# Kernel optimization log

Measured on AMD Instinct MI355X. Metric: run time of the kernel, lower is better.

The kernel has to match this reference:

```python
import jax, jax.numpy as jnp
import numpy as np

FM = 128       # feature_maps
QM = 128       # query_maps
ROUNDS = 4     # test_rounds (training=False)
N_VARS = 24576
N_CLAUSES = 98304
N_EDGES = 3 * N_CLAUSES
EPS = 1e-6


def _dense(k, fan_in, fan_out):
    return jax.random.normal(k, (fan_in, fan_out), jnp.float32) * (1.0 / np.sqrt(fan_in))


def setup_inputs() -> dict:
    key = jax.random.key(0)
    ks = jax.random.split(key, 20)
    return {
        "edge_lit": jax.random.randint(ks[0], (N_EDGES,), 0, 2 * N_VARS, dtype=jnp.int32),
        "edge_clause": jnp.sort(jax.random.randint(ks[1], (N_EDGES,), 0, N_CLAUSES, dtype=jnp.int32)),
        "noise_v": jax.random.normal(ks[2], (ROUNDS, N_VARS, 4), jnp.float32),
        "noise_c": jax.random.normal(ks[3], (ROUNDS, N_CLAUSES, 4), jnp.float32),
        # variables_query: MLP(2, QM, QM), input FM+4
        "vq_w0": _dense(ks[4], FM + 4, QM), "vq_b0": jnp.zeros((QM,), jnp.float32),
        "vq_w1": _dense(ks[5], QM, QM),     "vq_b1": jnp.zeros((QM,), jnp.float32),
        # clauses_query: MLP(2, QM, QM), input FM+4
        "cq_w0": _dense(ks[6], FM + 4, QM), "cq_b0": jnp.zeros((QM,), jnp.float32),
        "cq_w1": _dense(ks[7], QM, QM),     "cq_b1": jnp.zeros((QM,), jnp.float32),
        # clause_update: MLP(2, 2*FM, FM+QM), input FM+2*QM=384
        "cm_w0": _dense(ks[8], FM + 2 * QM, 2 * FM), "cm_b0": jnp.zeros((2 * FM,), jnp.float32),
        "cm_w1": _dense(ks[9], 2 * FM, FM + QM),     "cm_b1": jnp.zeros((FM + QM,), jnp.float32),
        # update_gate: MLP(3, 2*FM, FM), input QM+FM+2*QM=512
        "ug_w0": _dense(ks[10], QM + FM + 2 * QM, 2 * FM), "ug_b0": jnp.zeros((2 * FM,), jnp.float32),
        "ug_w1": _dense(ks[11], 2 * FM, 2 * FM),           "ug_b1": jnp.zeros((2 * FM,), jnp.float32),
        "ug_w2": _dense(ks[12], 2 * FM, FM),               "ug_b2": jnp.zeros((FM,), jnp.float32),
        # clauses_mask_output: MLP(2, FM, 1)
        "co_w0": _dense(ks[13], FM, FM), "co_b0": jnp.zeros((FM,), jnp.float32),
        "co_w1": _dense(ks[14], FM, 1),  "co_b1": jnp.zeros((1,), jnp.float32),
        "n_vars": N_VARS,
        "n_clauses": N_CLAUSES,
    }


def _forward(edge_lit, edge_clause, n_vars, n_clauses, floats):
    (noise_v, noise_c,
     vq_w0, vq_b0, vq_w1, vq_b1,
     cq_w0, cq_b0, cq_w1, cq_b1,
     cm_w0, cm_b0, cm_w1, cm_b1,
     ug_w0, ug_b0, ug_w1, ug_b1, ug_w2, ug_b2,
     co_w0, co_b0, co_w1, co_b1) = floats

    n_edges = edge_lit.shape[0]
    # lit_degree = row sums of sparse adjacency (all nonzeros are 1.0)
    lit_degree = jax.ops.segment_sum(jnp.ones((n_edges,), jnp.float32), edge_lit,
                                     num_segments=2 * n_vars)[:, None]          # [2V,1]
    degree_weight = jax.lax.rsqrt(jnp.maximum(lit_degree, 1.0))
    var_degree_weight = 4.0 * jax.lax.rsqrt(
        jnp.maximum(lit_degree[:n_vars] + lit_degree[n_vars:], 1.0))            # [V,1]

    def mlp2(x, w0, b0, w1, b1):
        return jax.nn.relu(x @ w0 + b0) @ w1 + b1

    def mlp3(x, w0, b0, w1, b1, w2, b2):
        h = jax.nn.relu(x @ w0 + b0)
        h = jax.nn.relu(h @ w1 + b1)
        return h @ w2 + b2

    def pair_norm(x):
        # PairNorm(subtract_mean=True), single graph -> global mean over nodes
        x = x - jnp.mean(x, axis=0, keepdims=True)
        return x * jax.lax.rsqrt(jnp.mean(jnp.square(x)) + EPS)

    def clauses_loss_fn(vq, cq):
        # unsat_cnf_clauses_loss: softplus literal values aggregated per clause,
        # clause satisfiability exp(-sum), gated by clause query mask.
        lits = jax.nn.softplus(jnp.concatenate([vq, -vq], axis=0))              # [2V,Q]
        csum = jax.ops.segment_sum(lits[edge_lit], edge_clause,
                                   num_segments=n_clauses)                      # [C,Q]
        loss = jnp.exp(-csum) * jax.nn.sigmoid(cq)
        return jnp.mean(loss), loss

    grad_fn = jax.grad(clauses_loss_fn, argnums=(0, 1), has_aux=True)

    def step(carry, xs):
        variables, clauses = carry
        nv, nc = xs
        vq = mlp2(jnp.concatenate([variables, nv], -1), vq_w0, vq_b0, vq_w1, vq_b1)
        cq = mlp2(jnp.concatenate([clauses, nc], -1), cq_w0, cq_b0, cq_w1, cq_b1)
        (vgrad, cgrad), clauses_loss = grad_fn(vq, cq)
        vgrad = vgrad * var_degree_weight
        clauses_loss = clauses_loss * 4.0
        clause_data = mlp2(jnp.concatenate([clauses, clauses_loss, cgrad], -1),
                           cm_w0, cm_b0, cm_w1, cm_b1)                          # [C,FM+QM]
        variables_loss_all = clause_data[:, :QM]
        clauses = pair_norm(clause_data[:, QM:]) * 0.25 + 0.1 * clauses
        # adj_matrix @ variables_loss_all (literal-side aggregation)
        variables_loss = jax.ops.segment_sum(variables_loss_all[edge_clause], edge_lit,
                                             num_segments=2 * n_vars) * degree_weight
        unit = jnp.concatenate([vgrad, variables,
                                variables_loss[:n_vars], variables_loss[n_vars:]], -1)
        variables = pair_norm(mlp3(unit, ug_w0, ug_b0, ug_w1, ug_b1, ug_w2, ug_b2)) * 0.25 \
                    + 0.1 * variables
        logits = mlp2(clauses, co_w0, co_b0, co_w1, co_b1)[:, 0]                # [C]
        return (variables, clauses), logits

    init = (jnp.ones((n_vars, FM), jnp.float32), jnp.ones((n_clauses, FM), jnp.float32))
    _, logits = jax.lax.scan(step, init, (noise_v, noise_c))                    # [R,C]
    return jax.nn.sigmoid(logits), jax.nn.softplus(logits)


def reference(edge_lit, edge_clause, noise_v, noise_c,
              vq_w0, vq_b0, vq_w1, vq_b1,
              cq_w0, cq_b0, cq_w1, cq_b1,
              cm_w0, cm_b0, cm_w1, cm_b1,
              ug_w0, ug_b0, ug_w1, ug_b1, ug_w2, ug_b2,
              co_w0, co_b0, co_w1, co_b1,
              n_vars, n_clauses):
    floats = (noise_v, noise_c,
              vq_w0, vq_b0, vq_w1, vq_b1,
              cq_w0, cq_b0, cq_w1, cq_b1,
              cm_w0, cm_b0, cm_w1, cm_b1,
              ug_w0, ug_b0, ug_w1, ug_b1, ug_w2, ug_b2,
              co_w0, co_b0, co_w1, co_b1)
    return _forward(edge_lit, edge_clause, int(n_vars), int(n_clauses), floats)
```

## Files before the change

### kernel.cpp

```cpp
#include <hip/hip_runtime.h>
#include <math.h>

#define NV 24576
#define NC 98304
#define NE 294912
#define CMCHUNK 24576

typedef unsigned short bf16;
typedef _Float16 f16;
using bf8 = __attribute__((ext_vector_type(8))) short;
using f4  = __attribute__((ext_vector_type(4))) float;

static constexpr float INV_CQM = 1.0f / 12582912.0f;
static constexpr float LOG2E = 1.44269504f;
static constexpr float LN2 = 0.69314718f;

__device__ __forceinline__ float b2f(bf16 h) { return __uint_as_float(((unsigned)h) << 16); }
__device__ __forceinline__ bf16 f2b(float f) {
  unsigned u = __float_as_uint(f);
  u += 0x7fff + ((u >> 16) & 1);
  return (bf16)(u >> 16);
}
__device__ __forceinline__ float fexp2(float x) { float r; asm("v_exp_f32 %0, %1" : "=v"(r) : "v"(x)); return r; }
__device__ __forceinline__ float flog2(float x) { float r; asm("v_log_f32 %0, %1" : "=v"(r) : "v"(x)); return r; }
__device__ __forceinline__ float frcpf(float x) { float r; asm("v_rcp_f32 %0, %1" : "=v"(r) : "v"(x)); return r; }
__device__ __forceinline__ float fsigm(float x) { return frcpf(1.0f + fexp2(-x * LOG2E)); }
__device__ __forceinline__ float fsoftplus(float x) {
  return fmaxf(x, 0.0f) + LN2 * flog2(1.0f + fexp2(-fabsf(x) * LOG2E));
}
__device__ __forceinline__ float cvt_ld(float x) { return x; }
__device__ __forceinline__ float cvt_ld(bf16 x) { return b2f(x); }

__device__ __forceinline__ void gload16(const void* g, void* l) {
  __builtin_amdgcn_global_load_lds((const __attribute__((address_space(1))) unsigned int*)g,
                                   (__attribute__((address_space(3))) unsigned int*)l, 16, 0, 0);
}


__global__ __launch_bounds__(256) void k_cptr(const int* __restrict__ ec, int* __restrict__ ptr) {
  int c = blockIdx.x * 256 + threadIdx.x;
  if (c > NC) return;
  int lo = 0, hi = NE;
  while (lo < hi) { int mid = (lo + hi) >> 1; if (ec[mid] < c) lo = mid + 1; else hi = mid; }
  ptr[c] = lo;
}

__global__ __launch_bounds__(256) void k_litcnt(const int* __restrict__ el, int* __restrict__ cnt) {
  int e = blockIdx.x * 256 + threadIdx.x;
  atomicAdd(&cnt[el[e]], 1);
}

__global__ __launch_bounds__(1024) void k_scan(int* __restrict__ cnt, int* __restrict__ ptr) {
  __shared__ int wsum[16];
  __shared__ int carry_s;
  int tid = threadIdx.x, lane = tid & 63, w = tid >> 6;
  if (tid == 0) carry_s = 0;
  __syncthreads();
  for (int base = 0; base < 2 * NV; base += 1024) {
    int x = cnt[base + tid];
    int v = x;
#pragma unroll
    for (int off = 1; off < 64; off <<= 1) {
      int y = __shfl_up(v, off, 64);
      if (lane >= off) v += y;
    }
    if (lane == 63) wsum[w] = v;
    __syncthreads();
    int carry = carry_s;
    int wpre = 0;
    for (int i = 0; i < w; ++i) wpre += wsum[i];
    int excl = carry + wpre + (v - x);
    ptr[base + tid] = excl;
    cnt[base + tid] = excl;
    __syncthreads();
    if (tid == 1023) carry_s = carry + wpre + v;
  }
  __syncthreads();
  if (tid == 0) ptr[2 * NV] = carry_s;
}

__global__ __launch_bounds__(256) void k_fillsort(const int* __restrict__ el, const int* __restrict__ ec,
                                                  int* __restrict__ cur, int* __restrict__ lclause) {
  int e = blockIdx.x * 256 + threadIdx.x;
  int pos = atomicAdd(&cur[el[e]], 1);
  lclause[pos] = ec[e];
}

__global__ __launch_bounds__(256) void k_degree(const int* __restrict__ lptr, float* __restrict__ dw,
                                                float* __restrict__ vdw) {
  int l = blockIdx.x * 256 + threadIdx.x;
  if (l < 2 * NV) dw[l] = rsqrtf(fmaxf((float)(lptr[l + 1] - lptr[l]), 1.0f));
  if (l < NV) {
    int d = (lptr[l + 1] - lptr[l]) + (lptr[l + NV + 1] - lptr[l + NV]);
    vdw[l] = 4.0f * rsqrtf(fmaxf((float)d, 1.0f));
  }
}

__global__ __launch_bounds__(256) void k_init_v(float* __restrict__ variables, bf16* __restrict__ ugA) {
  int i = blockIdx.x * 256 + threadIdx.x;
  variables[i] = 1.0f;
  ugA[(size_t)(i >> 7) * 512 + 128 + (i & 127)] = 0x3F80;
}
__global__ __launch_bounds__(256) void k_init_c(bf16* __restrict__ cmA) {
  int i = blockIdx.x * 256 + threadIdx.x;
  cmA[(size_t)(i >> 7) * 256 + (i & 127)] = 0x3F80;
}

__global__ __launch_bounds__(256) void k_wt(const float* __restrict__ w, bf16* __restrict__ wt,
                                            int K, int N, int Kpad) {
  int idx = blockIdx.x * 256 + threadIdx.x;
  int n = idx / Kpad, k = idx % Kpad;
  if (n >= N) return;
  wt[idx] = (k < K) ? f2b(w[(size_t)k * N + n]) : (bf16)0;
}


struct GP {
  const bf16* A0; const bf16* A1; int lda;
  const float* noise; const bf16* WT; const float* Bv;
  void* o0; void* o1; int ldOut;
};

enum { AL_STD = 0, AL_NOISE = 1, AL_CM = 2 };

template <int KDIM, int AL, bool RELU, int OUT>
__device__ __forceinline__ void gemm_body(const GP g, int bx, char* smem) {
  constexpr int NT = KDIM / 64;
  const int tid = threadIdx.x;
  const int m0 = bx * 128;
  const int n0 = blockIdx.y * 128;
  const int lane = tid & 63;
  const int w = tid >> 6;
  const int wr = w >> 1, wc = w & 1;
  const int rl = (tid >> 3) & 7;
  const int cc = tid & 7;
  const int swzoff = (cc * 16) ^ (rl << 4);

  auto stage = [&](int t, int buf) {
    char* As = smem + buf * 32768;
    char* Bs = As + 16384;
    const int k0 = t * 64;
    if (AL == AL_NOISE && t == 2) {
      const int srow = tid >> 3, schunk = tid & 7;
#pragma unroll
      for (int it = 0; it < 4; ++it) {
        int row = srow + it * 32;
        alignas(16) bf16 tmp[8];
#pragma unroll
        for (int e = 0; e < 8; ++e) {
          int kk = schunk * 8 + e;
          tmp[e] = (kk < 4) ? f2b(g.noise[(size_t)(m0 + row) * 4 + kk]) : (bf16)0;
        }
        *reinterpret_cast<uint4*>(&As[row * 128 + ((schunk * 16) ^ ((row & 7) << 4))]) =
            *reinterpret_cast<uint4*>(tmp);
        int row0 = it * 32 + w * 8;
        gload16((const char*)(g.WT + (size_t)(n0 + row0 + rl) * KDIM + k0) + swzoff, Bs + row0 * 128);
      }
    } else {
      const bf16* Ap = g.A0;
      int co_ = k0;
      if (AL == AL_CM) {
        if (t >= 2 && t < 4) Ap = g.A1;
        if (t >= 2) co_ = k0 - 128;
      }
#pragma unroll
      for (int it = 0; it < 4; ++it) {
        int row0 = it * 32 + w * 8;
        int row = row0 + rl;
        gload16((const char*)(Ap + (size_t)(m0 + row) * g.lda + co_) + swzoff, As + row0 * 128);
        gload16((const char*)(g.WT + (size_t)(n0 + row) * KDIM + k0) + swzoff, Bs + row0 * 128);
      }
    }
  };

  f4 acc[4][4] = {};
  stage(0, 0);
#pragma unroll
  for (int t = 0; t < NT; ++t) {
    const int buf = t & 1;
    __builtin_amdgcn_sched_barrier(0);
    if (t + 1 < NT) {
      stage(t + 1, buf ^ 1);
      if (AL == AL_NOISE && t + 1 == 2) {
        asm volatile("s_waitcnt vmcnt(4) lgkmcnt(0)" ::: "memory");
      } else {
        asm volatile("s_waitcnt vmcnt(8) lgkmcnt(0)" ::: "memory");
      }
    } else {
      asm volatile("s_waitcnt vmcnt(0) lgkmcnt(0)" ::: "memory");
    }
    __builtin_amdgcn_s_barrier();
    __builtin_amdgcn_sched_barrier(0);
    const char* As = smem + buf * 32768;
    const char* Bs = As + 16384;
#pragma unroll
    for (int kk = 0; kk < 2; ++kk) {
      bf8 a[4], b[4];
#pragma unroll
      for (int i = 0; i < 4; ++i) {
        int r = wr * 64 + i * 16 + (lane & 15);
        int cby = (kk * 64 + ((lane >> 4) * 16)) ^ ((r & 7) << 4);
        a[i] = *reinterpret_cast<const bf8*>(&As[r * 128 + cby]);
        int c = wc * 64 + i * 16 + (lane & 15);
        int cby2 = (kk * 64 + ((lane >> 4) * 16)) ^ ((c & 7) << 4);
        b[i] = *reinterpret_cast<const bf8*>(&Bs[c * 128 + cby2]);
      }
#pragma unroll
      for (int i = 0; i < 4; ++i)
#pragma unroll
        for (int j = 0; j < 4; ++j)
          acc[i][j] = __builtin_amdgcn_mfma_f32_16x16x32_bf16(a[i], b[j], acc[i][j], 0, 0, 0);
    }
    __builtin_amdgcn_sched_barrier(0);
    __builtin_amdgcn_s_barrier();
  }
  const int colloc = wc * 64 + (lane & 15);
  const int rowbase = m0 + wr * 64 + ((lane >> 4) << 2);

  if constexpr (OUT == 4) {
    const float* w1 = (const float*)g.o1;
    float* outp = (float*)g.o0;
    const int t = g.ldOut;
    float part[4][4];
#pragma unroll
    for (int i = 0; i < 4; ++i)
#pragma unroll
      for (int p = 0; p < 4; ++p) part[i][p] = 0.0f;
#pragma unroll
    for (int j = 0; j < 4; ++j) {
      int c = colloc + j * 16;
      float bias = g.Bv[c];
      float w1c = w1[c];
#pragma unroll
      for (int i = 0; i < 4; ++i)
#pragma unroll
        for (int p = 0; p < 4; ++p)
          part[i][p] += fmaxf(acc[i][j][p] + bias, 0.0f) * w1c;
    }
#pragma unroll
    for (int m = 1; m < 16; m <<= 1)
#pragma unroll
      for (int i = 0; i < 4; ++i)
#pragma unroll
        for (int p = 0; p < 4; ++p)
          part[i][p] += __shfl_xor(part[i][p], m, 64);
    float* red = (float*)smem;
    if ((lane & 15) == 0) {
#pragma unroll
      for (int i = 0; i < 4; ++i)
#pragma unroll
        for (int p = 0; p < 4; ++p)
          red[wc * 128 + wr * 64 + i * 16 + ((lane >> 4) << 2) + p] = part[i][p];
    }
    __syncthreads();
    if (tid < 128) {
      float lg = red[tid] + red[128 + tid] + g.noise[0];
      int row = m0 + tid;
      outp[(size_t)t * NC + row] = fsigm(lg);
      outp[(size_t)4 * NC + (size_t)t * NC + row] = fsoftplus(lg);
    }
    return;
  }

#pragma unroll
  for (int j = 0; j < 4; ++j) {
    int c = n0 + colloc + j * 16;
    float bias = g.Bv[c];
#pragma unroll
    for (int i = 0; i < 4; ++i) {
      int rb = rowbase + i * 16;
#pragma unroll
      for (int p = 0; p < 4; ++p) {
        float v = acc[i][j][p] + bias;
        if (RELU) v = fmaxf(v, 0.0f);
        int r = rb + p;
        if constexpr (OUT == 0) {
          ((float*)g.o0)[(size_t)r * g.ldOut + c] = v;
        } else if constexpr (OUT == 1) {
          ((bf16*)g.o0)[(size_t)r * g.ldOut + c] = f2b(v);
        } else if constexpr (OUT == 2) {
          if (c < 128) ((bf16*)g.o0)[(size_t)r * 256 + c] = f2b(v);
          else ((bf16*)g.o1)[(size_t)r * 128 + (c - 128)] = f2b(v);
        } else {
          float tq = LN2 * flog2(1.0f + fexp2(-fabsf(v) * LOG2E));
          ((f16*)g.o0)[(size_t)r * 128 + c] = (f16)(fmaxf(v, 0.0f) + tq);
          ((f16*)g.o1)[(size_t)r * 128 + c] = (f16)(fmaxf(-v, 0.0f) + tq);
        }
      }
    }
  }
}

template <int KDIM, int AL, bool RELU, int OUT>
__global__ __launch_bounds__(256) void mgemm_s(GP g) {
  __shared__ __align__(16) char smem[65536];
  gemm_body<KDIM, AL, RELU, OUT>(g, blockIdx.x, smem);
}

template <int KDIM, int AL, bool RELU, int OUTA, int OUTB>
__global__ __launch_bounds__(256) void mgemm_d(GP ga, GP gb, int nA) {
  __shared__ __align__(16) char smem[65536];
  if ((int)blockIdx.x < nA) gemm_body<KDIM, AL, RELU, OUTA>(ga, blockIdx.x, smem);
  else gemm_body<KDIM, AL, RELU, OUTB>(gb, blockIdx.x - nA, smem);
}


__global__ __launch_bounds__(256) void k_loss(const int* __restrict__ edge_lit, const int* __restrict__ cptr,
                                              const f16* __restrict__ sp, bf16* __restrict__ gbuf,
                                              bf16* __restrict__ cmA) {
  const int g = threadIdx.x >> 7;
  const int q = threadIdx.x & 127;
  const int c0 = blockIdx.x * 16 + g * 8;
#pragma unroll
  for (int ci = 0; ci < 8; ++ci) {
    int c = c0 + ci;
    int e0 = cptr[c], e1 = cptr[c + 1];
    float csum = 0.0f;
    for (int e = e0; e < e1; e += 4) {
#pragma unroll
      for (int k = 0; k < 4; ++k) {
        int ee = e + k;
        bool ok = ee < e1;
        int lit = ok ? edge_lit[ee] : 0;
        float v = ok ? (float)sp[(size_t)lit * 128 + q] : 0.0f;
        csum += v;
      }
    }
    float s = fsigm(b2f(gbuf[(size_t)c * 256 + 128 + q]));
    float L = fexp2(-csum * LOG2E) * s;
    gbuf[(size_t)c * 256 + q] = f2b(4.0f * L);
    cmA[(size_t)c * 256 + 128 + q] = f2b(L * (1.0f - s) * INV_CQM);
  }
}

__global__ __launch_bounds__(256) void k_gatherv(const int* __restrict__ lptr, const int* __restrict__ lclause,
                                                 const bf16* __restrict__ gbuf, const f16* __restrict__ spn,
                                                 const float* __restrict__ dw, const float* __restrict__ vdw,
                                                 bf16* __restrict__ ugA) {
  int v = blockIdx.x;
  int half = threadIdx.x >> 7, q = threadIdx.x & 127;
  int l = v + half * NV;
  int j0 = lptr[l], j1 = lptr[l + 1];
  float sg = 0.0f, sv = 0.0f;
  for (int j = j0; j < j1; j += 4) {
#pragma unroll
    for (int k = 0; k < 4; ++k) {
      int jj = j + k;
      bool ok = jj < j1;
      int c = ok ? lclause[jj] : 0;
      float a = ok ? b2f(gbuf[(size_t)c * 256 + q]) : 0.0f;
      float b = ok ? b2f(gbuf[(size_t)c * 256 + 128 + q]) : 0.0f;
      sg += a;
      sv += b;
    }
  }
  __shared__ float sgl[2][128];
  sgl[half][q] = sg;
  ugA[(size_t)v * 512 + 256 + half * 128 + q] = f2b(sv * dw[l]);
  __syncthreads();
  if (half == 0) {
    float s = fexp2(-LOG2E * (float)spn[(size_t)v * 128 + q]);
    float g = ((1.0f - s) * sgl[1][q] - s * sgl[0][q]) * (INV_CQM * 0.25f) * vdw[v];
    ugA[(size_t)v * 512 + q] = f2b(g);
  }
}

template <typename T>
__global__ __launch_bounds__(256) void k_pn_stats(const T* __restrict__ X, int R, float* __restrict__ stats) {
  int q = threadIdx.x & 127;
  int rg = threadIdx.x >> 7;
  float cs = 0.0f, ss = 0.0f;
  for (int r = blockIdx.x * 2 + rg; r < R; r += gridDim.x * 2) {
    float x = cvt_ld(X[(size_t)r * 128 + q]);
    cs += x;
    ss += x * x;
  }
  __shared__ float scs[256], sss[256];
  scs[threadIdx.x] = cs;
  sss[threadIdx.x] = ss;
  __syncthreads();
  if (threadIdx.x < 128) atomicAdd(&stats[q], scs[q] + scs[128 + q]);
  for (int off = 128; off; off >>= 1) {
    if (threadIdx.x < off) sss[threadIdx.x] += sss[threadIdx.x + off];
    __syncthreads();
  }
  if (threadIdx.x == 0) atomicAdd(&stats[128], sss[0]);
}

__global__ __launch_bounds__(128) void k_pn_final(float* __restrict__ stats, float R) {
  __shared__ float s[128];
  int q = threadIdx.x;
  float m = stats[q] / R;
  s[q] = m * m;
  __syncthreads();
  for (int off = 64; off; off >>= 1) {
    if (q < off) s[q] += s[q + off];
    __syncthreads();
  }
  if (q == 0) {
    float var = (stats[128] - R * s[0]) / (R * 128.0f);
    stats[129] = rsqrtf(fmaxf(var, 0.0f) + 1e-6f) * 0.25f;
  }
  stats[q] = m;
}

__global__ __launch_bounds__(256) void k_pn_apply_c(const bf16* __restrict__ cd1, const float* __restrict__ stats,
                                                    bf16* __restrict__ cmA) {
  int i = blockIdx.x * 256 + threadIdx.x;
  int c = i >> 7, q = i & 127;
  float x = b2f(cd1[i]);
  float old = b2f(cmA[(size_t)c * 256 + q]);
  cmA[(size_t)c * 256 + q] = f2b((x - stats[q]) * stats[129] + 0.1f * old);
}

__global__ __launch_bounds__(256) void k_pn_apply_v(const float* __restrict__ uout, const float* __restrict__ stats,
                                                    float* __restrict__ variables, bf16* __restrict__ ugA) {
  int i = blockIdx.x * 256 + threadIdx.x;
  int v = i >> 7, q = i & 127;
  float nv = (uout[i] - stats[q]) * stats[129] + 0.1f * variables[i];
  variables[i] = nv;
  ugA[(size_t)v * 512 + 128 + q] = f2b(nv);
}


extern "C" void kernel_launch(void* const* d_in, const int* in_sizes, int n_in,
                              void* d_out, int out_size, void* d_ws, size_t ws_size,
                              hipStream_t stream) {
  const int* edge_lit = (const int*)d_in[0];
  const int* edge_clause = (const int*)d_in[1];
  const float* noise_v = (const float*)d_in[2];
  const float* noise_c = (const float*)d_in[3];
  const float* vq_w0 = (const float*)d_in[4];  const float* vq_b0 = (const float*)d_in[5];
  const float* vq_w1 = (const float*)d_in[6];  const float* vq_b1 = (const float*)d_in[7];
  const float* cq_w0 = (const float*)d_in[8];  const float* cq_b0 = (const float*)d_in[9];
  const float* cq_w1 = (const float*)d_in[10]; const float* cq_b1 = (const float*)d_in[11];
  const float* cm_w0 = (const float*)d_in[12]; const float* cm_b0 = (const float*)d_in[13];
  const float* cm_w1 = (const float*)d_in[14]; const float* cm_b1 = (const float*)d_in[15];
  const float* ug_w0 = (const float*)d_in[16]; const float* ug_b0 = (const float*)d_in[17];
  const float* ug_w1 = (const float*)d_in[18]; const float* ug_b1 = (const float*)d_in[19];
  const float* ug_w2 = (const float*)d_in[20]; const float* ug_b2 = (const float*)d_in[21];
  const float* co_w0 = (const float*)d_in[22]; const float* co_b0 = (const float*)d_in[23];
  const float* co_w1 = (const float*)d_in[24]; const float* co_b1 = (const float*)d_in[25];
  float* out = (float*)d_out;

  char* base = (char*)d_ws;
  size_t off = 0;
  auto A = [&](size_t n) -> char* {
    char* p = base + off;
    off = (off + n + 255) & ~(size_t)255;
    return p;
  };
  float* variables = (float*)A((size_t)NV * 128 * 4);
  bf16* cmA        = (bf16*)A((size_t)NC * 256 * 2);
  bf16* gbuf       = (bf16*)A((size_t)NC * 256 * 2);
  bf16* ugA        = (bf16*)A((size_t)NV * 512 * 2);
  char* R_h        = A((size_t)NC * 128 * 2);
  char* R_big      = A((size_t)2 * NV * 128 * 2 + (size_t)NV * 128 * 4);
  bf16* wtb        = (bf16*)A(983424);
  int* cptr = (int*)A((size_t)(NC + 1) * 4);
  int* lptr = (int*)A((size_t)(2 * NV + 1) * 4);
  int* lcur = (int*)A((size_t)2 * NV * 4);
  int* lclause = (int*)A((size_t)NE * 4);
  float* dw  = (float*)A((size_t)2 * NV * 4);
  float* vdw = (float*)A((size_t)NV * 4);
  float* stats = (float*)A(2048);
  if (off > ws_size) {
    hipMemsetAsync(d_out, 0xFF, (size_t)out_size * 4, stream);
    return;
  }

  bf16* hc  = (bf16*)R_h;
  bf16* cd1 = (bf16*)R_h;
  bf16* uh1 = (bf16*)R_h;
  bf16* uh2 = (bf16*)(R_h + (size_t)NV * 256 * 2);
  bf16* hv  = (bf16*)R_big;
  bf16* cmh = (bf16*)R_big;
  f16* spp  = (f16*)(R_big + 12582912);
  f16* spn  = spp + (size_t)NV * 128;
  float* uout = (float*)(R_big + 12582912);

  size_t wo = 0;
  auto WTa = [&](int n, int kp) { bf16* p = wtb + wo; wo += (size_t)n * kp; return p; };
  bf16* wt_vq0 = WTa(128, 192); bf16* wt_vq1 = WTa(128, 128);
  bf16* wt_cq0 = WTa(128, 192); bf16* wt_cq1 = WTa(128, 128);
  bf16* wt_cm0 = WTa(256, 384); bf16* wt_cm1 = WTa(256, 256);
  bf16* wt_ug0 = WTa(256, 512); bf16* wt_ug1 = WTa(256, 256);
  bf16* wt_ug2 = WTa(128, 256); bf16* wt_co0 = WTa(128, 128);

  hipMemsetAsync(lcur, 0, (size_t)2 * NV * 4, stream);
  k_cptr<<<(NC + 256) / 256, 256, 0, stream>>>(edge_clause, cptr);
  k_litcnt<<<NE / 256, 256, 0, stream>>>(edge_lit, lcur);
  k_scan<<<1, 1024, 0, stream>>>(lcur, lptr);
  k_fillsort<<<NE / 256, 256, 0, stream>>>(edge_lit, edge_clause, lcur, lclause);
  k_degree<<<(2 * NV + 255) / 256, 256, 0, stream>>>(lptr, dw, vdw);
  k_init_v<<<NV * 128 / 256, 256, 0, stream>>>(variables, ugA);
  k_init_c<<<NC * 128 / 256, 256, 0, stream>>>(cmA);
  k_wt<<<128 * 192 / 256, 256, 0, stream>>>(vq_w0, wt_vq0, 132, 128, 192);
  k_wt<<<128 * 128 / 256, 256, 0, stream>>>(vq_w1, wt_vq1, 128, 128, 128);
  k_wt<<<128 * 192 / 256, 256, 0, stream>>>(cq_w0, wt_cq0, 132, 128, 192);
  k_wt<<<128 * 128 / 256, 256, 0, stream>>>(cq_w1, wt_cq1, 128, 128, 128);
  k_wt<<<256 * 384 / 256, 256, 0, stream>>>(cm_w0, wt_cm0, 384, 256, 384);
  k_wt<<<256 * 256 / 256, 256, 0, stream>>>(cm_w1, wt_cm1, 256, 256, 256);
  k_wt<<<256 * 512 / 256, 256, 0, stream>>>(ug_w0, wt_ug0, 512, 256, 512);
  k_wt<<<256 * 256 / 256, 256, 0, stream>>>(ug_w1, wt_ug1, 256, 256, 256);
  k_wt<<<128 * 256 / 256, 256, 0, stream>>>(ug_w2, wt_ug2, 256, 128, 256);
  k_wt<<<128 * 128 / 256, 256, 0, stream>>>(co_w0, wt_co0, 128, 128, 128);

  for (int t = 0; t < 4; ++t) {
    const float* nvp = noise_v + (size_t)t * NV * 4;
    const float* ncp = noise_c + (size_t)t * NC * 4;
    {
      GP pa{ugA + 128, nullptr, 512, nvp, wt_vq0, vq_b0, hv, nullptr, 128};
      GP pb{cmA, nullptr, 256, ncp, wt_cq0, cq_b0, hc, nullptr, 128};
      mgemm_d<192, AL_NOISE, true, 1, 1><<<dim3(960, 1), 256, 0, stream>>>(pa, pb, 192);
    }
    {
      GP pa{hv, nullptr, 128, nullptr, wt_vq1, vq_b1, spp, spn, 128};
      GP pb{hc, nullptr, 128, nullptr, wt_cq1, cq_b1, gbuf + 128, nullptr, 256};
      mgemm_d<128, AL_STD, false, 3, 1><<<dim3(960, 1), 256, 0, stream>>>(pa, pb, 192);
    }
    k_loss<<<NC / 16, 256, 0, stream>>>(edge_lit, cptr, spp, gbuf, cmA);
    for (int ch = 0; ch < NC / CMCHUNK; ++ch) {
      size_t ro = (size_t)ch * CMCHUNK;
      GP p0{cmA + ro * 256, gbuf + ro * 256, 256, nullptr, wt_cm0, cm_b0, cmh, nullptr, 256};
      mgemm_s<384, AL_CM, true, 1><<<dim3(CMCHUNK / 128, 2), 256, 0, stream>>>(p0);
      GP p1{cmh, nullptr, 256, nullptr, wt_cm1, cm_b1, gbuf + ro * 256 + 128, cd1 + ro * 128, 0};
      mgemm_s<256, AL_STD, false, 2><<<dim3(CMCHUNK / 128, 2), 256, 0, stream>>>(p1);
    }
    k_gatherv<<<NV, 256, 0, stream>>>(lptr, lclause, gbuf, spn, dw, vdw, ugA);
    hipMemsetAsync(stats, 0, 132 * 4, stream);
    k_pn_stats<bf16><<<256, 256, 0, stream>>>(cd1, NC, stats);
    k_pn_final<<<1, 128, 0, stream>>>(stats, (float)NC);
    k_pn_apply_c<<<NC * 128 / 256, 256, 0, stream>>>(cd1, stats, cmA);
    {
      GP p{cmA, nullptr, 256, co_b1, wt_co0, co_b0, out, (void*)co_w1, t};
      mgemm_s<128, AL_STD, false, 4><<<dim3(NC / 128, 1), 256, 0, stream>>>(p);
    }
    {
      GP p{ugA, nullptr, 512, nullptr, wt_ug0, ug_b0, uh1, nullptr, 256};
      mgemm_s<512, AL_STD, true, 1><<<dim3(NV / 128, 2), 256, 0, stream>>>(p);
    }
    {
      GP p{uh1, nullptr, 256, nullptr, wt_ug1, ug_b1, uh2, nullptr, 256};
      mgemm_s<256, AL_STD, true, 1><<<dim3(NV / 128, 2), 256, 0, stream>>>(p);
    }
    {
      GP p{uh2, nullptr, 256, nullptr, wt_ug2, ug_b2, uout, nullptr, 128};
      mgemm_s<256, AL_STD, false, 0><<<dim3(NV / 128, 1), 256, 0, stream>>>(p);
    }
    hipMemsetAsync(stats, 0, 132 * 4, stream);
    k_pn_stats<float><<<256, 256, 0, stream>>>(uout, NV, stats);
    k_pn_final<<<1, 128, 0, stream>>>(stats, (float)NV);
    k_pn_apply_v<<<NV * 128 / 256, 256, 0, stream>>>(uout, stats, variables, ugA);
  }
}
```

Baseline: 1.903 ms.

## Fuse pair-norm statistics into GEMM epilogues and enlarge clause-MLP chunks

Pair-norm column sums and sum of squares are now accumulated in the epilogue of the producing GEMMs, using wave shuffles, LDS atomics and global atomics. This removes the separate stats kernels and their memsets, and k_pn_final now zeroes the raw accumulators for the next use. It also doubles the clause-MLP chunk size so fewer launches are needed, and raises per-thread memory parallelism in k_loss (two clauses interleaved) and k_gatherv (unroll 8). The costs are extra atomic traffic and work in the GEMM epilogue, and a larger intermediate buffer reshuffled so that uout now aliases cmh.

New measurement: 1.689 ms. -11.2%, faster.

```diff
diff --git a/kernel.cpp b/kernel.cpp
--- a/kernel.cpp
+++ b/kernel.cpp
@@ -4,7 +4,7 @@
 #define NV 24576
 #define NC 98304
 #define NE 294912
-#define CMCHUNK 24576
+#define CMCHUNK 49152
 
 typedef unsigned short bf16;
 typedef _Float16 f16;
@@ -28,8 +28,6 @@
 __device__ __forceinline__ float fsoftplus(float x) {
   return fmaxf(x, 0.0f) + LN2 * flog2(1.0f + fexp2(-fabsf(x) * LOG2E));
 }
-__device__ __forceinline__ float cvt_ld(float x) { return x; }
-__device__ __forceinline__ float cvt_ld(bf16 x) { return b2f(x); }
 
 __device__ __forceinline__ void gload16(const void* g, void* l) {
   __builtin_amdgcn_global_load_lds((const __attribute__((address_space(1))) unsigned int*)g,
@@ -119,11 +117,12 @@
   const bf16* A0; const bf16* A1; int lda;
   const float* noise; const bf16* WT; const float* Bv;
   void* o0; void* o1; int ldOut;
+  float* stats;
 };
 
 enum { AL_STD = 0, AL_NOISE = 1, AL_CM = 2 };
 
-template <int KDIM, int AL, bool RELU, int OUT>
+template <int KDIM, int AL, bool RELU, int OUT, bool STAT = false>
 __device__ __forceinline__ void gemm_body(const GP g, int bx, char* smem) {
   constexpr int NT = KDIM / 64;
   const int tid = threadIdx.x;
@@ -262,6 +261,10 @@
     return;
   }
 
+  float colpart[4] = {0.0f, 0.0f, 0.0f, 0.0f};
+  float sq = 0.0f;
+  const bool statact = STAT && (OUT == 0 || n0 == 128);
+
 #pragma unroll
   for (int j = 0; j < 4; ++j) {
     int c = n0 + colloc + j * 16;
@@ -274,6 +277,9 @@
         float v = acc[i][j][p] + bias;
         if (RELU) v = fmaxf(v, 0.0f);
         int r = rb + p;
+        if constexpr (STAT) {
+          if (statact) { colpart[j] += v; sq += v * v; }
+        }
         if constexpr (OUT == 0) {
           ((float*)g.o0)[(size_t)r * g.ldOut + c] = v;
         } else if constexpr (OUT == 1) {
@@ -289,12 +295,36 @@
       }
     }
   }
-}
-
-template <int KDIM, int AL, bool RELU, int OUT>
+
+  if constexpr (STAT) {
+    if (statact) {
+#pragma unroll
+      for (int m = 16; m <= 32; m <<= 1)
+#pragma unroll
+        for (int j = 0; j < 4; ++j)
+          colpart[j] += __shfl_xor(colpart[j], m, 64);
+#pragma unroll
+      for (int m = 1; m <= 32; m <<= 1) sq += __shfl_xor(sq, m, 64);
+      float* csl = (float*)smem;
+      if (tid <= 128) csl[tid] = 0.0f;
+      __syncthreads();
+      if ((lane & 48) == 0) {
+#pragma unroll
+        for (int j = 0; j < 4; ++j)
+          atomicAdd(&csl[wc * 64 + (lane & 15) + j * 16], colpart[j]);
+      }
+      if (lane == 0) atomicAdd(&csl[128], sq);
+      __syncthreads();
+      if (tid < 128) atomicAdd(&g.stats[tid], csl[tid]);
+      else if (tid == 128) atomicAdd(&g.stats[128], csl[128]);
+    }
+  }
+}
+
+template <int KDIM, int AL, bool RELU, int OUT, bool STAT = false>
 __global__ __launch_bounds__(256) void mgemm_s(GP g) {
   __shared__ __align__(16) char smem[65536];
-  gemm_body<KDIM, AL, RELU, OUT>(g, blockIdx.x, smem);
+  gemm_body<KDIM, AL, RELU, OUT, STAT>(g, blockIdx.x, smem);
 }
 
 template <int KDIM, int AL, bool RELU, int OUTA, int OUTB>
@@ -312,24 +342,35 @@
   const int q = threadIdx.x & 127;
   const int c0 = blockIdx.x * 16 + g * 8;
 #pragma unroll
-  for (int ci = 0; ci < 8; ++ci) {
-    int c = c0 + ci;
-    int e0 = cptr[c], e1 = cptr[c + 1];
-    float csum = 0.0f;
-    for (int e = e0; e < e1; e += 4) {
+  for (int ci = 0; ci < 4; ++ci) {
+    int ca = c0 + ci * 2;
+    int e0a = cptr[ca], e1a = cptr[ca + 1], e1b = cptr[ca + 2];
+    int e0b = e1a;
+    float csa = 0.0f, csb = 0.0f;
+    int na = e1a - e0a, nb = e1b - e0b;
+    int nm = na > nb ? na : nb;
+    for (int b = 0; b < nm; b += 4) {
 #pragma unroll
       for (int k = 0; k < 4; ++k) {
-        int ee = e + k;
-        bool ok = ee < e1;
-        int lit = ok ? edge_lit[ee] : 0;
-        float v = ok ? (float)sp[(size_t)lit * 128 + q] : 0.0f;
-        csum += v;
-      }
-    }
-    float s = fsigm(b2f(gbuf[(size_t)c * 256 + 128 + q]));
-    float L = fexp2(-csum * LOG2E) * s;
-    gbuf[(size_t)c * 256 + q] = f2b(4.0f * L);
-    cmA[(size_t)c * 256 + 128 + q] = f2b(L * (1.0f - s) * INV_CQM);
+        int ea = e0a + b + k;
+        bool oka = ea < e1a;
+        int la = oka ? edge_lit[ea] : 0;
+        csa += oka ? (float)sp[(size_t)la * 128 + q] : 0.0f;
+        int eb = e0b + b + k;
+        bool okb = eb < e1b;
+        int lb = okb ? edge_lit[eb] : 0;
+        csb += okb ? (float)sp[(size_t)lb * 128 + q] : 0.0f;
+      }
+    }
+    float s = fsigm(b2f(gbuf[(size_t)ca * 256 + 128 + q]));
+    float L = fexp2(-csa * LOG2E) * s;
+    gbuf[(size_t)ca * 256 + q] = f2b(4.0f * L);
+    cmA[(size_t)ca * 256 + 128 + q] = f2b(L * (1.0f - s) * INV_CQM);
+    int cb = ca + 1;
+    float s2 = fsigm(b2f(gbuf[(size_t)cb * 256 + 128 + q]));
+    float L2 = fexp2(-csb * LOG2E) * s2;
+    gbuf[(size_t)cb * 256 + q] = f2b(4.0f * L2);
+    cmA[(size_t)cb * 256 + 128 + q] = f2b(L2 * (1.0f - s2) * INV_CQM);
   }
 }
 
@@ -342,9 +383,9 @@
   int l = v + half * NV;
   int j0 = lptr[l], j1 = lptr[l + 1];
   float sg = 0.0f, sv = 0.0f;
-  for (int j = j0; j < j1; j += 4) {
-#pragma unroll
-    for (int k = 0; k < 4; ++k) {
+  for (int j = j0; j < j1; j += 8) {
+#pragma unroll
+    for (int k = 0; k < 8; ++k) {
       int jj = j + k;
       bool ok = jj < j1;
       int c = ok ? lclause[jj] : 0;
@@ -365,32 +406,10 @@
   }
 }
 
-template <typename T>
-__global__ __launch_bounds__(256) void k_pn_stats(const T* __restrict__ X, int R, float* __restrict__ stats) {
-  int q = threadIdx.x & 127;
-  int rg = threadIdx.x >> 7;
-  float cs = 0.0f, ss = 0.0f;
-  for (int r = blockIdx.x * 2 + rg; r < R; r += gridDim.x * 2) {
-    float x = cvt_ld(X[(size_t)r * 128 + q]);
-    cs += x;
-    ss += x * x;
-  }
-  __shared__ float scs[256], sss[256];
-  scs[threadIdx.x] = cs;
-  sss[threadIdx.x] = ss;
-  __syncthreads();
-  if (threadIdx.x < 128) atomicAdd(&stats[q], scs[q] + scs[128 + q]);
-  for (int off = 128; off; off >>= 1) {
-    if (threadIdx.x < off) sss[threadIdx.x] += sss[threadIdx.x + off];
-    __syncthreads();
-  }
-  if (threadIdx.x == 0) atomicAdd(&stats[128], sss[0]);
-}
-
-__global__ __launch_bounds__(128) void k_pn_final(float* __restrict__ stats, float R) {
+__global__ __launch_bounds__(128) void k_pn_final(float* __restrict__ raw, float* __restrict__ outp, float R) {
   __shared__ float s[128];
   int q = threadIdx.x;
-  float m = stats[q] / R;
+  float m = raw[q] / R;
   s[q] = m * m;
   __syncthreads();
   for (int off = 64; off; off >>= 1) {
@@ -398,26 +417,28 @@
     __syncthreads();
   }
   if (q == 0) {
-    float var = (stats[128] - R * s[0]) / (R * 128.0f);
-    stats[129] = rsqrtf(fmaxf(var, 0.0f) + 1e-6f) * 0.25f;
-  }
-  stats[q] = m;
-}
-
-__global__ __launch_bounds__(256) void k_pn_apply_c(const bf16* __restrict__ cd1, const float* __restrict__ stats,
+    float var = (raw[128] - R * s[0]) / (R * 128.0f);
+    outp[128] = rsqrtf(fmaxf(var, 0.0f) + 1e-6f) * 0.25f;
+    raw[128] = 0.0f;
+  }
+  outp[q] = m;
+  raw[q] = 0.0f;
+}
+
+__global__ __launch_bounds__(256) void k_pn_apply_c(const bf16* __restrict__ cd1, const float* __restrict__ st,
                                                     bf16* __restrict__ cmA) {
   int i = blockIdx.x * 256 + threadIdx.x;
   int c = i >> 7, q = i & 127;
   float x = b2f(cd1[i]);
   float old = b2f(cmA[(size_t)c * 256 + q]);
-  cmA[(size_t)c * 256 + q] = f2b((x - stats[q]) * stats[129] + 0.1f * old);
-}
-
-__global__ __launch_bounds__(256) void k_pn_apply_v(const float* __restrict__ uout, const float* __restrict__ stats,
+  cmA[(size_t)c * 256 + q] = f2b((x - st[q]) * st[128] + 0.1f * old);
+}
+
+__global__ __launch_bounds__(256) void k_pn_apply_v(const float* __restrict__ uout, const float* __restrict__ st,
                                                     float* __restrict__ variables, bf16* __restrict__ ugA) {
   int i = blockIdx.x * 256 + threadIdx.x;
   int v = i >> 7, q = i & 127;
-  float nv = (uout[i] - stats[q]) * stats[129] + 0.1f * variables[i];
+  float nv = (uout[i] - st[q]) * st[128] + 0.1f * variables[i];
   variables[i] = nv;
   ugA[(size_t)v * 512 + 128 + q] = f2b(nv);
 }
@@ -455,7 +476,7 @@
   bf16* gbuf       = (bf16*)A((size_t)NC * 256 * 2);
   bf16* ugA        = (bf16*)A((size_t)NV * 512 * 2);
   char* R_h        = A((size_t)NC * 128 * 2);
-  char* R_big      = A((size_t)2 * NV * 128 * 2 + (size_t)NV * 128 * 4);
+  char* R_big      = A((size_t)CMCHUNK * 256 * 2 + (size_t)2 * NV * 128 * 2);
   bf16* wtb        = (bf16*)A(983424);
   int* cptr = (int*)A((size_t)(NC + 1) * 4);
   int* lptr = (int*)A((size_t)(2 * NV + 1) * 4);
@@ -468,6 +489,7 @@
     hipMemsetAsync(d_out, 0xFF, (size_t)out_size * 4, stream);
     return;
   }
+  float* statsOut = stats + 256;
 
   bf16* hc  = (bf16*)R_h;
   bf16* cd1 = (bf16*)R_h;
@@ -475,9 +497,9 @@
   bf16* uh2 = (bf16*)(R_h + (size_t)NV * 256 * 2);
   bf16* hv  = (bf16*)R_big;
   bf16* cmh = (bf16*)R_big;
-  f16* spp  = (f16*)(R_big + 12582912);
+  float* uout = (float*)R_big;
+  f16* spp  = (f16*)(R_big + (size_t)CMCHUNK * 256 * 2);
   f16* spn  = spp + (size_t)NV * 128;
-  float* uout = (float*)(R_big + 12582912);
 
   size_t wo = 0;
   auto WTa = [&](int n, int kp) { bf16* p = wtb + wo; wo += (size_t)n * kp; return p; };
@@ -488,6 +510,7 @@
   bf16* wt_ug2 = WTa(128, 256); bf16* wt_co0 = WTa(128, 128);
 
   hipMemsetAsync(lcur, 0, (size_t)2 * NV * 4, stream);
+  hipMemsetAsync(stats, 0, 1024, stream);
   k_cptr<<<(NC + 256) / 256, 256, 0, stream>>>(edge_clause, cptr);
   k_litcnt<<<NE / 256, 256, 0, stream>>>(edge_lit, lcur);
   k_scan<<<1, 1024, 0, stream>>>(lcur, lptr);
@@ -524,14 +547,12 @@
       size_t ro = (size_t)ch * CMCHUNK;
       GP p0{cmA + ro * 256, gbuf + ro * 256, 256, nullptr, wt_cm0, cm_b0, cmh, nullptr, 256};
       mgemm_s<384, AL_CM, true, 1><<<dim3(CMCHUNK / 128, 2), 256, 0, stream>>>(p0);
-      GP p1{cmh, nullptr, 256, nullptr, wt_cm1, cm_b1, gbuf + ro * 256 + 128, cd1 + ro * 128, 0};
-      mgemm_s<256, AL_STD, false, 2><<<dim3(CMCHUNK / 128, 2), 256, 0, stream>>>(p1);
+      GP p1{cmh, nullptr, 256, nullptr, wt_cm1, cm_b1, gbuf + ro * 256 + 128, cd1 + ro * 128, 0, stats};
+      mgemm_s<256, AL_STD, false, 2, true><<<dim3(CMCHUNK / 128, 2), 256, 0, stream>>>(p1);
     }
     k_gatherv<<<NV, 256, 0, stream>>>(lptr, lclause, gbuf, spn, dw, vdw, ugA);
-    hipMemsetAsync(stats, 0, 132 * 4, stream);
-    k_pn_stats<bf16><<<256, 256, 0, stream>>>(cd1, NC, stats);
-    k_pn_final<<<1, 128, 0, stream>>>(stats, (float)NC);
-    k_pn_apply_c<<<NC * 128 / 256, 256, 0, stream>>>(cd1, stats, cmA);
+    k_pn_final<<<1, 128, 0, stream>>>(stats, statsOut, (float)NC);
+    k_pn_apply_c<<<NC * 128 / 256, 256, 0, stream>>>(cd1, statsOut, cmA);
     {
       GP p{cmA, nullptr, 256, co_b1, wt_co0, co_b0, out, (void*)co_w1, t};
       mgemm_s<128, AL_STD, false, 4><<<dim3(NC / 128, 1), 256, 0, stream>>>(p);
@@ -545,12 +566,10 @@
       mgemm_s<256, AL_STD, true, 1><<<dim3(NV / 128, 2), 256, 0, stream>>>(p);
     }
     {
-      GP p{uh2, nullptr, 256, nullptr, wt_ug2, ug_b2, uout, nullptr, 128};
-      mgemm_s<256, AL_STD, false, 0><<<dim3(NV / 128, 1), 256, 0, stream>>>(p);
-    }
-    hipMemsetAsync(stats, 0, 132 * 4, stream);
-    k_pn_stats<float><<<256, 256, 0, stream>>>(uout, NV, stats);
-    k_pn_final<<<1, 128, 0, stream>>>(stats, (float)NV);
-    k_pn_apply_v<<<NV * 128 / 256, 256, 0, stream>>>(uout, stats, variables, ugA);
-  }
-}
+      GP p{uh2, nullptr, 256, nullptr, wt_ug2, ug_b2, uout, nullptr, 128, stats};
+      mgemm_s<256, AL_STD, false, 0, true><<<dim3(NV / 128, 1), 256, 0, stream>>>(p);
+    }
+    k_pn_final<<<1, 128, 0, stream>>>(stats, statsOut, (float)NV);
+    k_pn_apply_v<<<NV * 128 / 256, 256, 0, stream>>>(uout, statsOut, variables, ugA);
+  }
+}
```
